# Performance work log

Hardware: AMD Instinct MI355X
Metric: run time of the kernel (lower is better)

Reference implementation:

```python
import jax, jax.numpy as jnp
import numpy as np

N, E, G = 50000, 600000, 64
F_NODE, F_EDGE, F_HAD = 20, 4, 12
D, H, C, L = 128, 4, 32, 3  # hidden, heads, per-head channels, num_layers


def setup_inputs() -> dict:
    key = jax.random.key(0)
    ks = iter(jax.random.split(key, 64))
    nrm = lambda shp, s=0.1: jax.random.normal(next(ks), shp, dtype=jnp.float32) * s
    inp = {
        'x': jax.random.normal(next(ks), (N, F_NODE), dtype=jnp.float32),
        'edge_attr': jax.random.normal(next(ks), (E, F_EDGE), dtype=jnp.float32),
        'haddock_features': jax.random.normal(next(ks), (G, F_HAD), dtype=jnp.float32),
        'edge_index': jax.random.randint(next(ks), (2, E), 0, N, dtype=jnp.int64),
        'batch': (jnp.arange(N, dtype=jnp.int64) * G) // N,  # sorted, all graphs non-empty
        # node embed
        'embed_w': nrm((F_NODE, D)), 'embed_b': jnp.zeros((D,), jnp.float32),
        # GAT layers (stacked over L)
        'gat_lin_w': nrm((L, D, H * C)),
        'gat_att_src': nrm((L, H, C)), 'gat_att_dst': nrm((L, H, C)),
        'gat_edge_w': nrm((L, F_EDGE, H * C)), 'gat_att_edge': nrm((L, H, C)),
        'gat_bias': jnp.zeros((L, H * C), jnp.float32),
        'ln_g': jnp.ones((L, D), jnp.float32), 'ln_b': jnp.zeros((L, D), jnp.float32),
        # haddock processor
        'had_w1': nrm((F_HAD, D)), 'had_b1': jnp.zeros((D,), jnp.float32),
        'had_w2': nrm((D, D)), 'had_b2': jnp.zeros((D,), jnp.float32),
        # interaction head (in = 3*D)
        'int_w1': nrm((3 * D, D)), 'int_b1': jnp.zeros((D,), jnp.float32),
        'int_w2': nrm((D, 64)), 'int_b2': jnp.zeros((64,), jnp.float32),
        'int_w3': nrm((64, 1)), 'int_b3': jnp.zeros((1,), jnp.float32),
        # binding affinity head
        'aff_w1': nrm((3 * D, D)), 'aff_b1': jnp.zeros((D,), jnp.float32),
        'aff_w2': nrm((D, 64)), 'aff_b2': jnp.zeros((64,), jnp.float32),
        'aff_w3': nrm((64, 1)), 'aff_b3': jnp.zeros((1,), jnp.float32),
        # MultiheadAttention with seq_len=1: softmax over 1 key == 1, so output
        # reduces exactly to out_proj(v_proj(x)); q/k projections cancel.
        'mha_v_w': nrm((D, D)), 'mha_v_b': jnp.zeros((D,), jnp.float32),
        'mha_o_w': nrm((D, D)), 'mha_o_b': jnp.zeros((D,), jnp.float32),
    }
    return inp


def _layernorm(x, g, b, eps=1e-5):
    mu = jnp.mean(x, axis=-1, keepdims=True)
    var = jnp.var(x, axis=-1, keepdims=True)
    return (x - mu) * jax.lax.rsqrt(var + eps) * g + b


def _gat_layer(x, src, dst, edge_attr, lin_w, a_src, a_dst, edge_w, a_edge, bias):
    n = x.shape[0]
    h = (x @ lin_w).reshape(n, H, C)                      # [N,H,C]
    alpha_s = jnp.sum(h * a_src, axis=-1)                 # [N,H]
    alpha_d = jnp.sum(h * a_dst, axis=-1)                 # [N,H]
    eemb = (edge_attr @ edge_w).reshape(-1, H, C)         # [E,H,C]
    alpha_e = jnp.sum(eemb * a_edge, axis=-1)             # [E,H]
    alpha = alpha_s[src] + alpha_d[dst] + alpha_e         # [E,H]
    alpha = jax.nn.leaky_relu(alpha, 0.2)
    m = jax.ops.segment_max(alpha, dst, num_segments=n)
    m = jnp.where(jnp.isfinite(m), m, 0.0)
    ex = jnp.exp(alpha - m[dst])
    denom = jax.ops.segment_sum(ex, dst, num_segments=n)
    w = ex / (denom[dst] + 1e-16)                         # segment softmax over dst
    msg = h[src] * w[:, :, None]                          # [E,H,C]
    out = jax.ops.segment_sum(msg, dst, num_segments=n)   # [N,H,C]
    return out.reshape(n, H * C) + bias


def reference(x, edge_attr, haddock_features, embed_w, embed_b,
              gat_lin_w, gat_att_src, gat_att_dst, gat_edge_w, gat_att_edge, gat_bias,
              ln_g, ln_b, had_w1, had_b1, had_w2, had_b2,
              int_w1, int_b1, int_w2, int_b2, int_w3, int_b3,
              aff_w1, aff_b1, aff_w2, aff_b2, aff_w3, aff_b3,
              mha_v_w, mha_v_b, mha_o_w, mha_o_b, edge_index, batch):
    src, dst = edge_index[0], edge_index[1]
    h = jax.nn.relu(x @ embed_w + embed_b)
    for i in range(L):
        res = h
        h = _gat_layer(h, src, dst, edge_attr, gat_lin_w[i], gat_att_src[i],
                       gat_att_dst[i], gat_edge_w[i], gat_att_edge[i], gat_bias[i])
        h = jax.nn.relu(_layernorm(h + res, ln_g[i], ln_b[i]))  # dropout = identity (eval)
    counts = jax.ops.segment_sum(jnp.ones((h.shape[0],), h.dtype), batch, num_segments=G)
    g_mean = jax.ops.segment_sum(h, batch, num_segments=G) / counts[:, None]
    g_max = jax.ops.segment_max(h, batch, num_segments=G)
    graph_embed = jnp.concatenate([g_mean, g_max], axis=1)      # [G,2D]
    had = jax.nn.relu(haddock_features @ had_w1 + had_b1) @ had_w2 + had_b2
    comb = jnp.concatenate([graph_embed, had], axis=1)          # [G,3D]
    z = jax.nn.relu(comb @ int_w1 + int_b1)
    z = jax.nn.relu(z @ int_w2 + int_b2)
    interaction = jax.nn.sigmoid(z @ int_w3 + int_b3)[:, 0]
    z = jax.nn.relu(comb @ aff_w1 + aff_b1)
    z = jax.nn.relu(z @ aff_w2 + aff_b2)
    affinity = (z @ aff_w3 + aff_b3)[:, 0]
    # self-attention over seq_len=1: weights==1, output = out_proj(v_proj(x))
    attn = (h @ mha_v_w + mha_v_b) @ mha_o_w + mha_o_b
    return interaction, affinity, attn, h
```

## Files before the change

### kernel.cpp

```cpp
#include <hip/hip_runtime.h>
#include <hip/hip_bf16.h>

typedef float v4 __attribute__((ext_vector_type(4)));
typedef float f32x4 __attribute__((ext_vector_type(4)));
typedef short bf16x8 __attribute__((ext_vector_type(8)));
typedef unsigned short us8 __attribute__((ext_vector_type(8)));

__device__ __forceinline__ unsigned short f2bf(float f) {
    unsigned u = __float_as_uint(f);
    u = (u + 0x7FFFu + ((u >> 16) & 1u)) >> 16;
    return (unsigned short)u;
}
__device__ __forceinline__ float bf2f(unsigned short s) {
    return __uint_as_float(((unsigned)s) << 16);
}

__global__ __launch_bounds__(256) void k_embed(const float* __restrict__ x,
                                               const float* __restrict__ w,
                                               const float* __restrict__ b,
                                               float* __restrict__ h,
                                               unsigned short* __restrict__ h_bf, int n) {
    int idx = blockIdx.x * 256 + threadIdx.x;
    if (idx >= n * 128) return;
    int node = idx >> 7, j = idx & 127;
    float acc = b[j];
#pragma unroll
    for (int k = 0; k < 20; ++k) acc += x[node * 20 + k] * w[k * 128 + j];
    float r = fmaxf(acc, 0.f);
    h[idx] = r;
    h_bf[idx] = f2bf(r);
}


__global__ __launch_bounds__(256) void k_csr_zero(int* __restrict__ cnt,
                                                  int* __restrict__ cursor, int n) {
    int i = blockIdx.x * 256 + threadIdx.x;
    if (i < n) { cnt[i] = 0; cursor[i] = 0; }
}

__global__ __launch_bounds__(256) void k_hist(const int* __restrict__ ei,
                                              int* __restrict__ cnt, int E_) {
    int e = blockIdx.x * 256 + threadIdx.x;
    if (e < E_) atomicAdd(&cnt[ei[E_ + e]], 1);
}

__global__ __launch_bounds__(256) void k_scan_local(const int* __restrict__ cnt,
                                                    int* __restrict__ ptr,
                                                    int* __restrict__ bsum, int n) {
    __shared__ int s[256];
    int t = threadIdx.x, i = blockIdx.x * 256 + t;
    int v = (i < n) ? cnt[i] : 0;
    s[t] = v;
    __syncthreads();
    for (int o = 1; o < 256; o <<= 1) {
        int x = (t >= o) ? s[t - o] : 0;
        __syncthreads();
        s[t] += x;
        __syncthreads();
    }
    if (i < n) ptr[i] = s[t] - v;
    if (t == 255) bsum[blockIdx.x] = s[255];
}

__global__ __launch_bounds__(256) void k_scan_bsum(int* __restrict__ bsum, int nb) {
    __shared__ int s[256];
    int t = threadIdx.x;
    int v = (t < nb) ? bsum[t] : 0;
    s[t] = v;
    __syncthreads();
    for (int o = 1; o < 256; o <<= 1) {
        int x = (t >= o) ? s[t - o] : 0;
        __syncthreads();
        s[t] += x;
        __syncthreads();
    }
    if (t < nb) bsum[t] = s[t] - v;
}

__global__ __launch_bounds__(256) void k_scan_add(int* __restrict__ ptr,
                                                  const int* __restrict__ bsum,
                                                  int n, int E_) {
    int i = blockIdx.x * 256 + threadIdx.x;
    if (i < n) ptr[i] += bsum[i >> 8];
    if (i == 0) ptr[n] = E_;
}

__global__ __launch_bounds__(256) void k_scatter(const int* __restrict__ ei,
                                                 const float* __restrict__ edge_attr,
                                                 const int* __restrict__ ptr,
                                                 int* __restrict__ cursor,
                                                 int* __restrict__ esrc_s,
                                                 float* __restrict__ ea_s, int E_) {
    int e = blockIdx.x * 256 + threadIdx.x;
    if (e >= E_) return;
    int d = ei[E_ + e];
    int p = ptr[d] + atomicAdd(&cursor[d], 1);
    esrc_s[p] = ei[e];
    ((v4*)ea_s)[p] = ((const v4*)edge_attr)[e];
}

__global__ __launch_bounds__(128) void k_fuse_vo(const float* __restrict__ vw,
                                                 const float* __restrict__ vb,
                                                 const float* __restrict__ ow,
                                                 const float* __restrict__ ob,
                                                 float* __restrict__ Wc,
                                                 float* __restrict__ bc) {
    int k = blockIdx.x, j = threadIdx.x;
    float acc = 0.f;
    for (int m = 0; m < 128; ++m) acc += vw[k * 128 + m] * ow[m * 128 + j];
    Wc[k * 128 + j] = acc;
    if (k == 0) {
        float b = ob[j];
        for (int m = 0; m < 128; ++m) b += vb[m] * ow[m * 128 + j];
        bc[j] = b;
    }
}

__global__ __launch_bounds__(256) void k_pack_w(const float* __restrict__ gat_lin_w,
                                                const float* __restrict__ Wc,
                                                unsigned short* __restrict__ Bpack) {
    int m = blockIdx.y;
    const float* W = (m < 3) ? (gat_lin_w + (size_t)m * 16384) : Wc;
    int idx = blockIdx.x * 256 + threadIdx.x;
    int e = idx & 7, l = (idx >> 3) & 63, kb = (idx >> 9) & 3, c = idx >> 11;
    int k = kb * 32 + ((l >> 4) << 3) + e;
    int col = c * 16 + (l & 15);
    Bpack[(size_t)m * 16384 + idx] = f2bf(W[k * 128 + col]);
}

template <bool ALPHAS, bool OUTF32>
__global__ __launch_bounds__(256) void k_gemm_mfma(
    const unsigned short* __restrict__ A,
    const unsigned short* __restrict__ Bpack,
    const float* __restrict__ bias,
    unsigned short* __restrict__ out_bf,
    float* __restrict__ out_f32,
    const float* __restrict__ avs, const float* __restrict__ avd,
    float* __restrict__ asrc, float* __restrict__ adst, int nn) {
    __shared__ float lds[64][132];
    int tid = threadIdx.x;
    int w = tid >> 6, l = tid & 63;
    int row0 = blockIdx.x * 64;
    int arow = row0 + w * 16 + (l & 15);
    int koff = (l >> 4) * 8;

    bf16x8 a[4];
#pragma unroll
    for (int kb = 0; kb < 4; ++kb)
        a[kb] = *(const bf16x8*)&A[(size_t)arow * 128 + kb * 32 + koff];

    const bf16x8* bp = (const bf16x8*)Bpack;
    f32x4 acc[8];
#pragma unroll
    for (int c = 0; c < 8; ++c) {
        f32x4 z = {0.f, 0.f, 0.f, 0.f};
        acc[c] = z;
#pragma unroll
        for (int kb = 0; kb < 4; ++kb)
            acc[c] = __builtin_amdgcn_mfma_f32_16x16x32_bf16(a[kb], bp[(c * 4 + kb) * 64 + l],
                                                             acc[c], 0, 0, 0);
    }

    int colb = l & 15;
    int rowb = w * 16 + (l >> 4) * 4;
#pragma unroll
    for (int c = 0; c < 8; ++c)
#pragma unroll
        for (int r = 0; r < 4; ++r)
            lds[rowb + r][c * 16 + colb] = acc[c][r];
    __syncthreads();

    int rl = tid >> 2, q = tid & 3;
    int gr = row0 + rl;
    if (gr >= nn) return;
    float v[32];
#pragma unroll
    for (int j = 0; j < 8; ++j)
        *(f32x4*)&v[j * 4] = *(const f32x4*)&lds[rl][q * 32 + j * 4];

    if (ALPHAS) {
        float ps = 0.f, pd = 0.f;
#pragma unroll
        for (int j = 0; j < 32; ++j) {
            ps += v[j] * avs[q * 32 + j];
            pd += v[j] * avd[q * 32 + j];
        }
        asrc[(size_t)gr * 4 + q] = ps;
        adst[(size_t)gr * 4 + q] = pd;
    }
    if (OUTF32) {
#pragma unroll
        for (int j = 0; j < 32; ++j) v[j] += bias[q * 32 + j];
#pragma unroll
        for (int j = 0; j < 8; ++j)
            *(f32x4*)&out_f32[(size_t)gr * 128 + q * 32 + j * 4] = *(f32x4*)&v[j * 4];
    } else {
        us8 o0, o1;
#pragma unroll
        for (int j = 0; j < 8; ++j) o0[j] = f2bf(v[j]);
#pragma unroll
        for (int j = 0; j < 8; ++j) o1[j] = f2bf(v[8 + j]);
        *(us8*)&out_bf[(size_t)gr * 128 + q * 32] = o0;
        *(us8*)&out_bf[(size_t)gr * 128 + q * 32 + 8] = o1;
        us8 o2, o3;
#pragma unroll
        for (int j = 0; j < 8; ++j) o2[j] = f2bf(v[16 + j]);
#pragma unroll
        for (int j = 0; j < 8; ++j) o3[j] = f2bf(v[24 + j]);
        *(us8*)&out_bf[(size_t)gr * 128 + q * 32 + 16] = o2;
        *(us8*)&out_bf[(size_t)gr * 128 + q * 32 + 24] = o3;
    }
}

__global__ __launch_bounds__(256) void k_node_agg(
    const unsigned short* __restrict__ hl_bf, const int* __restrict__ ptr,
    const int* __restrict__ esrc_s, const float* __restrict__ ea_s,
    const float* __restrict__ asrc, const float* __restrict__ adst,
    const float* __restrict__ edge_w, const float* __restrict__ a_edge,
    const float* __restrict__ bias, const float* __restrict__ lng,
    const float* __restrict__ lnb, float* __restrict__ h,
    unsigned short* __restrict__ h_bf, int n) {
    __shared__ float aew[16];
    int tid = threadIdx.x;
    if (tid < 16) {
        int k = tid >> 2, hh = tid & 3;
        float s = 0.f;
        for (int c = 0; c < 32; ++c) s += edge_w[k * 128 + hh * 32 + c] * a_edge[hh * 32 + c];
        aew[tid] = s;
    }
    __syncthreads();

    int node = blockIdx.x * 4 + (tid >> 6);
    if (node >= n) return;
    int lane = tid & 63;
    int g = lane >> 4;
    int l16 = lane & 15;
    int c0 = l16 * 8;
    int hh = l16 >> 2;

    float aewc0 = aew[hh], aewc1 = aew[4 + hh], aewc2 = aew[8 + hh], aewc3 = aew[12 + hh];
    int start = ptr[node], end = ptr[node + 1];
    float adn = adst[(size_t)node * 4 + hh];

    float acc[8] = {};
    float den = 0.f;
    int p = start + g;
    int srcp = (p < end) ? esrc_s[p] : 0;
    for (; p < end; p += 4) {
        int srcn = (p + 4 < end) ? esrc_s[p + 4] : 0;
        v4 ea = ((const v4*)ea_s)[p];
        float a = asrc[(size_t)srcp * 4 + hh] + adn +
                  ea[0] * aewc0 + ea[1] * aewc1 + ea[2] * aewc2 + ea[3] * aewc3;
        a = a > 0.f ? a : 0.2f * a;
        float ex = __expf(a);
        den += ex;
        us8 hv = *(const us8*)&hl_bf[(size_t)srcp * 128 + c0];
#pragma unroll
        for (int j = 0; j < 8; ++j) acc[j] += ex * bf2f(hv[j]);
        srcp = srcn;
    }

#pragma unroll
    for (int j = 0; j < 8; ++j) {
        acc[j] += __shfl_xor(acc[j], 16);
        acc[j] += __shfl_xor(acc[j], 32);
    }
    den += __shfl_xor(den, 16);
    den += __shfl_xor(den, 32);

    float inv = 1.f / (den + 1e-16f);
    v4 r0 = *(const v4*)&h[(size_t)node * 128 + c0];
    v4 r1 = *(const v4*)&h[(size_t)node * 128 + c0 + 4];
    v4 b0 = *(const v4*)&bias[c0];
    v4 b1 = *(const v4*)&bias[c0 + 4];
    float v[8];
#pragma unroll
    for (int j = 0; j < 4; ++j) v[j] = acc[j] * inv + b0[j] + r0[j];
#pragma unroll
    for (int j = 0; j < 4; ++j) v[4 + j] = acc[4 + j] * inv + b1[j] + r1[j];

    float s = 0.f, sq = 0.f;
#pragma unroll
    for (int j = 0; j < 8; ++j) { s += v[j]; sq += v[j] * v[j]; }
#pragma unroll
    for (int o = 1; o < 16; o <<= 1) { s += __shfl_xor(s, o); sq += __shfl_xor(sq, o); }
    float mu = s * (1.f / 128.f);
    float var = sq * (1.f / 128.f) - mu * mu;
    float rs = rsqrtf(var + 1e-5f);

    if (g == 0) {
        v4 g0 = *(const v4*)&lng[c0];
        v4 g1 = *(const v4*)&lng[c0 + 4];
        v4 lb0 = *(const v4*)&lnb[c0];
        v4 lb1 = *(const v4*)&lnb[c0 + 4];
        v4 o0, o1;
#pragma unroll
        for (int j = 0; j < 4; ++j) o0[j] = fmaxf((v[j] - mu) * rs * g0[j] + lb0[j], 0.f);
#pragma unroll
        for (int j = 0; j < 4; ++j) o1[j] = fmaxf((v[4 + j] - mu) * rs * g1[j] + lb1[j], 0.f);
        *(v4*)&h[(size_t)node * 128 + c0] = o0;
        *(v4*)&h[(size_t)node * 128 + c0 + 4] = o1;
        us8 ob;
#pragma unroll
        for (int j = 0; j < 4; ++j) ob[j] = f2bf(o0[j]);
#pragma unroll
        for (int j = 0; j < 4; ++j) ob[4 + j] = f2bf(o1[j]);
        *(us8*)&h_bf[(size_t)node * 128 + c0] = ob;
    }
}

__device__ __forceinline__ int lower_bound_i(const int* a, int n, int key) {
    int lo = 0, hi = n;
    while (lo < hi) {
        int mid = (lo + hi) >> 1;
        if (a[mid] < key) lo = mid + 1; else hi = mid;
    }
    return lo;
}


__global__ __launch_bounds__(256) void k_pool_zero(float* __restrict__ gsum,
                                                   float* __restrict__ gmax, int g128) {
    int i = blockIdx.x * 256 + threadIdx.x;
    if (i < g128) { gsum[i] = 0.f; gmax[i] = 0.f; }
}

__global__ __launch_bounds__(256) void k_pool_part(const float* __restrict__ h,
                                                   const int* __restrict__ batch,
                                                   float* __restrict__ gsum,
                                                   float* __restrict__ gmax,
                                                   int n, int chunk) {
    int start = blockIdx.x * chunk;
    int end = min(start + chunk, n);
    if (start >= end) return;
    int j = threadIdx.x & 127, half = threadIdx.x >> 7;
    float s = 0.f, mx = 0.f;
    int curg = -1;
    for (int node = start + half; node < end; node += 2) {
        int g = batch[node];
        if (g != curg) {
            if (curg >= 0) {
                atomicAdd(&gsum[curg * 128 + j], s);
                atomicMax((int*)&gmax[curg * 128 + j], __float_as_int(mx));
            }
            curg = g; s = 0.f; mx = 0.f;
        }
        float v = h[(size_t)node * 128 + j];
        s += v;
        mx = fmaxf(mx, v);
    }
    if (curg >= 0) {
        atomicAdd(&gsum[curg * 128 + j], s);
        atomicMax((int*)&gmax[curg * 128 + j], __float_as_int(mx));
    }
}

__global__ __launch_bounds__(128) void k_pool_fin(const float* __restrict__ gsum,
                                                  const float* __restrict__ gmax,
                                                  const int* __restrict__ batch,
                                                  float* __restrict__ comb, int n) {
    int g = blockIdx.x, j = threadIdx.x;
    int start = lower_bound_i(batch, n, g);
    int end = lower_bound_i(batch, n, g + 1);
    float cnt = (float)(end - start);
    comb[g * 384 + j] = gsum[g * 128 + j] / cnt;
    comb[g * 384 + 128 + j] = gmax[g * 128 + j];
}

__global__ __launch_bounds__(128) void k_had(const float* __restrict__ hf,
                                             const float* __restrict__ w1,
                                             const float* __restrict__ b1,
                                             const float* __restrict__ w2,
                                             const float* __restrict__ b2,
                                             float* __restrict__ comb) {
    __shared__ float h1[128];
    int g = blockIdx.x, j = threadIdx.x;
    float acc = b1[j];
#pragma unroll
    for (int k = 0; k < 12; ++k) acc += hf[g * 12 + k] * w1[k * 128 + j];
    h1[j] = fmaxf(acc, 0.f);
    __syncthreads();
    float a2 = b2[j];
    for (int k = 0; k < 128; ++k) a2 += h1[k] * w2[k * 128 + j];
    comb[g * 384 + 256 + j] = a2;
}

__global__ __launch_bounds__(128) void k_head(const float* __restrict__ comb,
                                              const float* __restrict__ w1,
                                              const float* __restrict__ b1,
                                              const float* __restrict__ w2,
                                              const float* __restrict__ b2,
                                              const float* __restrict__ w3,
                                              const float* __restrict__ b3,
                                              float* __restrict__ outp, int sigm) {
    __shared__ float cs[384];
    __shared__ float z1[128];
    __shared__ float z2[64];
    int g = blockIdx.x, j = threadIdx.x;
    for (int k = j; k < 384; k += 128) cs[k] = comb[g * 384 + k];
    __syncthreads();
    float acc = b1[j];
    for (int k = 0; k < 384; ++k) acc += cs[k] * w1[k * 128 + j];
    z1[j] = fmaxf(acc, 0.f);
    __syncthreads();
    if (j < 64) {
        float a2 = b2[j];
        for (int k = 0; k < 128; ++k) a2 += z1[k] * w2[k * 64 + j];
        z2[j] = fmaxf(a2, 0.f);
    }
    __syncthreads();
    if (j == 0) {
        float a3 = b3[0];
        for (int k = 0; k < 64; ++k) a3 += z2[k] * w3[k];
        if (sigm) a3 = 1.f / (1.f + __expf(-a3));
        outp[g] = a3;
    }
}

extern "C" void kernel_launch(void* const* d_in, const int* in_sizes, int n_in,
                              void* d_out, int out_size, void* d_ws, size_t ws_size,
                              hipStream_t stream) {
    const float* x = (const float*)d_in[0];
    const float* edge_attr = (const float*)d_in[1];
    const float* haddock = (const float*)d_in[2];
    const int* ei = (const int*)d_in[3];
    const int* batch = (const int*)d_in[4];
    const float* embed_w = (const float*)d_in[5];
    const float* embed_b = (const float*)d_in[6];
    const float* gat_lin_w = (const float*)d_in[7];
    const float* gat_att_src = (const float*)d_in[8];
    const float* gat_att_dst = (const float*)d_in[9];
    const float* gat_edge_w = (const float*)d_in[10];
    const float* gat_att_edge = (const float*)d_in[11];
    const float* gat_bias = (const float*)d_in[12];
    const float* ln_g = (const float*)d_in[13];
    const float* ln_b = (const float*)d_in[14];
    const float* had_w1 = (const float*)d_in[15];
    const float* had_b1 = (const float*)d_in[16];
    const float* had_w2 = (const float*)d_in[17];
    const float* had_b2 = (const float*)d_in[18];
    const float* int_w1 = (const float*)d_in[19];
    const float* int_b1 = (const float*)d_in[20];
    const float* int_w2 = (const float*)d_in[21];
    const float* int_b2 = (const float*)d_in[22];
    const float* int_w3 = (const float*)d_in[23];
    const float* int_b3 = (const float*)d_in[24];
    const float* aff_w1 = (const float*)d_in[25];
    const float* aff_b1 = (const float*)d_in[26];
    const float* aff_w2 = (const float*)d_in[27];
    const float* aff_b2 = (const float*)d_in[28];
    const float* aff_w3 = (const float*)d_in[29];
    const float* aff_b3 = (const float*)d_in[30];
    const float* mha_v_w = (const float*)d_in[31];
    const float* mha_v_b = (const float*)d_in[32];
    const float* mha_o_w = (const float*)d_in[33];
    const float* mha_o_b = (const float*)d_in[34];

    const int N_ = in_sizes[0] / 20;
    const int E_ = in_sizes[1] / 4;
    const int G_ = in_sizes[2] / 12;
    const int Npad = (N_ + 63) & ~63;

    float* out_f = (float*)d_out;
    float* inter_out = out_f;
    float* aff_out = out_f + G_;
    float* attn_out = out_f + 2 * G_;
    float* h_buf = attn_out + (size_t)N_ * 128;

    unsigned short* h_bf = (unsigned short*)d_ws;
    unsigned short* hl_bf = h_bf + (size_t)Npad * 128;
    unsigned short* Bpack = hl_bf + (size_t)Npad * 128;
    float* ea_s = (float*)(Bpack + 4 * 16384);
    float* Wc = ea_s + (size_t)E_ * 4;
    float* bc = Wc + 16384;
    float* asrc = bc + 128;
    float* adst = asrc + (size_t)N_ * 4;
    float* gsum = adst + (size_t)N_ * 4;
    float* gmax = gsum + (size_t)G_ * 128;
    float* comb = gmax + (size_t)G_ * 128;
    int* cnt = (int*)(comb + (size_t)G_ * 384);
    int* cursor = cnt + N_;
    int* ptr = cursor + N_;
    int* bsum = ptr + N_ + 4;
    int* esrc_s = bsum + 256;

    const int nb_scan = (N_ + 255) / 256;
    const int POOL_BLOCKS = 2048;
    const int chunk = (N_ + POOL_BLOCKS - 1) / POOL_BLOCKS;
    const int gemm_blocks = (N_ + 63) / 64;

    k_embed<<<(N_ * 128 + 255) / 256, 256, 0, stream>>>(x, embed_w, embed_b, h_buf, h_bf, N_);

    k_csr_zero<<<nb_scan, 256, 0, stream>>>(cnt, cursor, N_);
    k_hist<<<(E_ + 255) / 256, 256, 0, stream>>>(ei, cnt, E_);
    k_scan_local<<<nb_scan, 256, 0, stream>>>(cnt, ptr, bsum, N_);
    k_scan_bsum<<<1, 256, 0, stream>>>(bsum, nb_scan);
    k_scan_add<<<nb_scan, 256, 0, stream>>>(ptr, bsum, N_, E_);
    k_scatter<<<(E_ + 255) / 256, 256, 0, stream>>>(ei, edge_attr, ptr, cursor,
                                                    esrc_s, ea_s, E_);

    k_fuse_vo<<<128, 128, 0, stream>>>(mha_v_w, mha_v_b, mha_o_w, mha_o_b, Wc, bc);
    k_pack_w<<<dim3(64, 4), 256, 0, stream>>>(gat_lin_w, Wc, Bpack);
    k_pool_zero<<<(G_ * 128 + 255) / 256, 256, 0, stream>>>(gsum, gmax, G_ * 128);

    for (int i = 0; i < 3; ++i) {
        k_gemm_mfma<true, false><<<gemm_blocks, 256, 0, stream>>>(
            h_bf, Bpack + (size_t)i * 16384, nullptr, hl_bf, nullptr,
            gat_att_src + i * 128, gat_att_dst + i * 128, asrc, adst, N_);
        k_node_agg<<<(N_ + 3) / 4, 256, 0, stream>>>(
            hl_bf, ptr, esrc_s, ea_s, asrc, adst,
            gat_edge_w + (size_t)i * 512, gat_att_edge + i * 128,
            gat_bias + i * 128, ln_g + i * 128, ln_b + i * 128, h_buf, h_bf, N_);
    }

    k_pool_part<<<POOL_BLOCKS, 256, 0, stream>>>(h_buf, batch, gsum, gmax, N_, chunk);
    k_pool_fin<<<G_, 128, 0, stream>>>(gsum, gmax, batch, comb, N_);
    k_had<<<G_, 128, 0, stream>>>(haddock, had_w1, had_b1, had_w2, had_b2, comb);
    k_head<<<G_, 128, 0, stream>>>(comb, int_w1, int_b1, int_w2, int_b2, int_w3, int_b3,
                                   inter_out, 1);
    k_head<<<G_, 128, 0, stream>>>(comb, aff_w1, aff_b1, aff_w2, aff_b2, aff_w3, aff_b3,
                                   aff_out, 0);
    k_gemm_mfma<false, true><<<gemm_blocks, 256, 0, stream>>>(
        h_bf, Bpack + (size_t)3 * 16384, bc, nullptr, attn_out,
        nullptr, nullptr, nullptr, nullptr, N_);
}
```

Baseline: 404.8 us.

## Widen node aggregation lanes, fuse graph head kernels, pool from bf16, use memsets

The node aggregation kernel now gives each lane 16 channels and runs 8 edge streams per node instead of 4, so each lane issues wider gathers and more edges are in flight. The pool-finish, haddock and two head kernels are merged into one graph-output kernel. Pooling now reads the bf16 copy of h, which halves its read traffic but may shift results slightly. The zeroing kernels are replaced with hipMemsetAsync, which cuts launch count.

```diff
diff --git a/kernel.cpp b/kernel.cpp
--- a/kernel.cpp
+++ b/kernel.cpp
@@ -31,12 +31,6 @@
     h_bf[idx] = f2bf(r);
 }
 
-
-__global__ __launch_bounds__(256) void k_csr_zero(int* __restrict__ cnt,
-                                                  int* __restrict__ cursor, int n) {
-    int i = blockIdx.x * 256 + threadIdx.x;
-    if (i < n) { cnt[i] = 0; cursor[i] = 0; }
-}
 
 __global__ __launch_bounds__(256) void k_hist(const int* __restrict__ ei,
                                               int* __restrict__ cnt, int E_) {
@@ -195,20 +189,14 @@
         for (int j = 0; j < 8; ++j)
             *(f32x4*)&out_f32[(size_t)gr * 128 + q * 32 + j * 4] = *(f32x4*)&v[j * 4];
     } else {
-        us8 o0, o1;
-#pragma unroll
-        for (int j = 0; j < 8; ++j) o0[j] = f2bf(v[j]);
-#pragma unroll
-        for (int j = 0; j < 8; ++j) o1[j] = f2bf(v[8 + j]);
-        *(us8*)&out_bf[(size_t)gr * 128 + q * 32] = o0;
-        *(us8*)&out_bf[(size_t)gr * 128 + q * 32 + 8] = o1;
-        us8 o2, o3;
-#pragma unroll
-        for (int j = 0; j < 8; ++j) o2[j] = f2bf(v[16 + j]);
-#pragma unroll
-        for (int j = 0; j < 8; ++j) o3[j] = f2bf(v[24 + j]);
-        *(us8*)&out_bf[(size_t)gr * 128 + q * 32 + 16] = o2;
-        *(us8*)&out_bf[(size_t)gr * 128 + q * 32 + 24] = o3;
+        us8 o[4];
+#pragma unroll
+        for (int t = 0; t < 4; ++t)
+#pragma unroll
+            for (int j = 0; j < 8; ++j) o[t][j] = f2bf(v[t * 8 + j]);
+#pragma unroll
+        for (int t = 0; t < 4; ++t)
+            *(us8*)&out_bf[(size_t)gr * 128 + q * 32 + t * 8] = o[t];
     }
 }
 
@@ -233,79 +221,86 @@
     int node = blockIdx.x * 4 + (tid >> 6);
     if (node >= n) return;
     int lane = tid & 63;
-    int g = lane >> 4;
-    int l16 = lane & 15;
-    int c0 = l16 * 8;
-    int hh = l16 >> 2;
+    int g = lane >> 3;
+    int l8 = lane & 7;
+    int c0 = l8 * 16;
+    int hh = l8 >> 1;
 
     float aewc0 = aew[hh], aewc1 = aew[4 + hh], aewc2 = aew[8 + hh], aewc3 = aew[12 + hh];
     int start = ptr[node], end = ptr[node + 1];
     float adn = adst[(size_t)node * 4 + hh];
 
-    float acc[8] = {};
+    float acc[16] = {};
     float den = 0.f;
     int p = start + g;
     int srcp = (p < end) ? esrc_s[p] : 0;
-    for (; p < end; p += 4) {
-        int srcn = (p + 4 < end) ? esrc_s[p + 4] : 0;
+    for (; p < end; p += 8) {
+        int srcn = (p + 8 < end) ? esrc_s[p + 8] : 0;
         v4 ea = ((const v4*)ea_s)[p];
+        us8 hv0 = *(const us8*)&hl_bf[(size_t)srcp * 128 + c0];
+        us8 hv1 = *(const us8*)&hl_bf[(size_t)srcp * 128 + c0 + 8];
         float a = asrc[(size_t)srcp * 4 + hh] + adn +
                   ea[0] * aewc0 + ea[1] * aewc1 + ea[2] * aewc2 + ea[3] * aewc3;
         a = a > 0.f ? a : 0.2f * a;
         float ex = __expf(a);
         den += ex;
-        us8 hv = *(const us8*)&hl_bf[(size_t)srcp * 128 + c0];
-#pragma unroll
-        for (int j = 0; j < 8; ++j) acc[j] += ex * bf2f(hv[j]);
+#pragma unroll
+        for (int j = 0; j < 8; ++j) acc[j] += ex * bf2f(hv0[j]);
+#pragma unroll
+        for (int j = 0; j < 8; ++j) acc[8 + j] += ex * bf2f(hv1[j]);
         srcp = srcn;
     }
 
 #pragma unroll
-    for (int j = 0; j < 8; ++j) {
+    for (int j = 0; j < 16; ++j) {
+        acc[j] += __shfl_xor(acc[j], 8);
         acc[j] += __shfl_xor(acc[j], 16);
         acc[j] += __shfl_xor(acc[j], 32);
     }
+    den += __shfl_xor(den, 8);
     den += __shfl_xor(den, 16);
     den += __shfl_xor(den, 32);
 
     float inv = 1.f / (den + 1e-16f);
-    v4 r0 = *(const v4*)&h[(size_t)node * 128 + c0];
-    v4 r1 = *(const v4*)&h[(size_t)node * 128 + c0 + 4];
-    v4 b0 = *(const v4*)&bias[c0];
-    v4 b1 = *(const v4*)&bias[c0 + 4];
-    float v[8];
-#pragma unroll
-    for (int j = 0; j < 4; ++j) v[j] = acc[j] * inv + b0[j] + r0[j];
-#pragma unroll
-    for (int j = 0; j < 4; ++j) v[4 + j] = acc[4 + j] * inv + b1[j] + r1[j];
+    float v[16];
+#pragma unroll
+    for (int t = 0; t < 4; ++t) {
+        v4 r = *(const v4*)&h[(size_t)node * 128 + c0 + t * 4];
+        v4 b = *(const v4*)&bias[c0 + t * 4];
+#pragma unroll
+        for (int j = 0; j < 4; ++j) v[t * 4 + j] = acc[t * 4 + j] * inv + b[j] + r[j];
+    }
 
     float s = 0.f, sq = 0.f;
 #pragma unroll
-    for (int j = 0; j < 8; ++j) { s += v[j]; sq += v[j] * v[j]; }
-#pragma unroll
-    for (int o = 1; o < 16; o <<= 1) { s += __shfl_xor(s, o); sq += __shfl_xor(sq, o); }
+    for (int j = 0; j < 16; ++j) { s += v[j]; sq += v[j] * v[j]; }
+#pragma unroll
+    for (int o = 1; o < 8; o <<= 1) { s += __shfl_xor(s, o); sq += __shfl_xor(sq, o); }
     float mu = s * (1.f / 128.f);
     float var = sq * (1.f / 128.f) - mu * mu;
     float rs = rsqrtf(var + 1e-5f);
 
     if (g == 0) {
-        v4 g0 = *(const v4*)&lng[c0];
-        v4 g1 = *(const v4*)&lng[c0 + 4];
-        v4 lb0 = *(const v4*)&lnb[c0];
-        v4 lb1 = *(const v4*)&lnb[c0 + 4];
-        v4 o0, o1;
-#pragma unroll
-        for (int j = 0; j < 4; ++j) o0[j] = fmaxf((v[j] - mu) * rs * g0[j] + lb0[j], 0.f);
-#pragma unroll
-        for (int j = 0; j < 4; ++j) o1[j] = fmaxf((v[4 + j] - mu) * rs * g1[j] + lb1[j], 0.f);
-        *(v4*)&h[(size_t)node * 128 + c0] = o0;
-        *(v4*)&h[(size_t)node * 128 + c0 + 4] = o1;
-        us8 ob;
-#pragma unroll
-        for (int j = 0; j < 4; ++j) ob[j] = f2bf(o0[j]);
-#pragma unroll
-        for (int j = 0; j < 4; ++j) ob[4 + j] = f2bf(o1[j]);
-        *(us8*)&h_bf[(size_t)node * 128 + c0] = ob;
+        float y[16];
+#pragma unroll
+        for (int t = 0; t < 4; ++t) {
+            v4 gg = *(const v4*)&lng[c0 + t * 4];
+            v4 lb = *(const v4*)&lnb[c0 + t * 4];
+            v4 o;
+#pragma unroll
+            for (int j = 0; j < 4; ++j) {
+                o[j] = fmaxf((v[t * 4 + j] - mu) * rs * gg[j] + lb[j], 0.f);
+                y[t * 4 + j] = o[j];
+            }
+            *(v4*)&h[(size_t)node * 128 + c0 + t * 4] = o;
+        }
+        us8 ob0, ob1;
+#pragma unroll
+        for (int j = 0; j < 8; ++j) ob0[j] = f2bf(y[j]);
+#pragma unroll
+        for (int j = 0; j < 8; ++j) ob1[j] = f2bf(y[8 + j]);
+        *(us8*)&h_bf[(size_t)node * 128 + c0] = ob0;
+        *(us8*)&h_bf[(size_t)node * 128 + c0 + 8] = ob1;
     }
 }
 
@@ -319,13 +314,7 @@
 }
 
 
-__global__ __launch_bounds__(256) void k_pool_zero(float* __restrict__ gsum,
-                                                   float* __restrict__ gmax, int g128) {
-    int i = blockIdx.x * 256 + threadIdx.x;
-    if (i < g128) { gsum[i] = 0.f; gmax[i] = 0.f; }
-}
-
-__global__ __launch_bounds__(256) void k_pool_part(const float* __restrict__ h,
+__global__ __launch_bounds__(256) void k_pool_part(const unsigned short* __restrict__ h_bf,
                                                    const int* __restrict__ batch,
                                                    float* __restrict__ gsum,
                                                    float* __restrict__ gmax,
@@ -333,87 +322,92 @@
     int start = blockIdx.x * chunk;
     int end = min(start + chunk, n);
     if (start >= end) return;
-    int j = threadIdx.x & 127, half = threadIdx.x >> 7;
-    float s = 0.f, mx = 0.f;
+    int c0 = (threadIdx.x & 63) * 2;
+    int strm = threadIdx.x >> 6;
+    float s0 = 0.f, s1 = 0.f, m0 = 0.f, m1 = 0.f;
     int curg = -1;
-    for (int node = start + half; node < end; node += 2) {
+    for (int node = start + strm; node < end; node += 4) {
         int g = batch[node];
         if (g != curg) {
             if (curg >= 0) {
-                atomicAdd(&gsum[curg * 128 + j], s);
-                atomicMax((int*)&gmax[curg * 128 + j], __float_as_int(mx));
+                atomicAdd(&gsum[curg * 128 + c0], s0);
+                atomicAdd(&gsum[curg * 128 + c0 + 1], s1);
+                atomicMax((int*)&gmax[curg * 128 + c0], __float_as_int(m0));
+                atomicMax((int*)&gmax[curg * 128 + c0 + 1], __float_as_int(m1));
             }
-            curg = g; s = 0.f; mx = 0.f;
+            curg = g; s0 = s1 = 0.f; m0 = m1 = 0.f;
         }
-        float v = h[(size_t)node * 128 + j];
-        s += v;
-        mx = fmaxf(mx, v);
+        unsigned u = *(const unsigned*)&h_bf[(size_t)node * 128 + c0];
+        float v0 = __uint_as_float(u << 16);
+        float v1 = __uint_as_float(u & 0xffff0000u);
+        s0 += v0; s1 += v1;
+        m0 = fmaxf(m0, v0); m1 = fmaxf(m1, v1);
     }
     if (curg >= 0) {
-        atomicAdd(&gsum[curg * 128 + j], s);
-        atomicMax((int*)&gmax[curg * 128 + j], __float_as_int(mx));
-    }
-}
-
-__global__ __launch_bounds__(128) void k_pool_fin(const float* __restrict__ gsum,
-                                                  const float* __restrict__ gmax,
-                                                  const int* __restrict__ batch,
-                                                  float* __restrict__ comb, int n) {
-    int g = blockIdx.x, j = threadIdx.x;
-    int start = lower_bound_i(batch, n, g);
-    int end = lower_bound_i(batch, n, g + 1);
-    float cnt = (float)(end - start);
-    comb[g * 384 + j] = gsum[g * 128 + j] / cnt;
-    comb[g * 384 + 128 + j] = gmax[g * 128 + j];
-}
-
-__global__ __launch_bounds__(128) void k_had(const float* __restrict__ hf,
-                                             const float* __restrict__ w1,
-                                             const float* __restrict__ b1,
-                                             const float* __restrict__ w2,
-                                             const float* __restrict__ b2,
-                                             float* __restrict__ comb) {
+        atomicAdd(&gsum[curg * 128 + c0], s0);
+        atomicAdd(&gsum[curg * 128 + c0 + 1], s1);
+        atomicMax((int*)&gmax[curg * 128 + c0], __float_as_int(m0));
+        atomicMax((int*)&gmax[curg * 128 + c0 + 1], __float_as_int(m1));
+    }
+}
+
+__global__ __launch_bounds__(256) void k_graph_out(
+    const float* __restrict__ gsum, const float* __restrict__ gmax,
+    const int* __restrict__ batch, const float* __restrict__ hf,
+    const float* __restrict__ had_w1, const float* __restrict__ had_b1,
+    const float* __restrict__ had_w2, const float* __restrict__ had_b2,
+    const float* __restrict__ int_w1, const float* __restrict__ int_b1,
+    const float* __restrict__ int_w2, const float* __restrict__ int_b2,
+    const float* __restrict__ int_w3, const float* __restrict__ int_b3,
+    const float* __restrict__ aff_w1, const float* __restrict__ aff_b1,
+    const float* __restrict__ aff_w2, const float* __restrict__ aff_b2,
+    const float* __restrict__ aff_w3, const float* __restrict__ aff_b3,
+    float* __restrict__ inter_out, float* __restrict__ aff_out, int n) {
+    __shared__ float comb[384];
     __shared__ float h1[128];
-    int g = blockIdx.x, j = threadIdx.x;
+    __shared__ float z1[2][128];
+    __shared__ float z2[2][64];
+    int g = blockIdx.x, tid = threadIdx.x;
+    if (tid < 128) {
+        int start = lower_bound_i(batch, n, g);
+        int end = lower_bound_i(batch, n, g + 1);
+        float cnt = (float)(end - start);
+        comb[tid] = gsum[g * 128 + tid] / cnt;
+        comb[128 + tid] = gmax[g * 128 + tid];
+        float acc = had_b1[tid];
+#pragma unroll
+        for (int k = 0; k < 12; ++k) acc += hf[g * 12 + k] * had_w1[k * 128 + tid];
+        h1[tid] = fmaxf(acc, 0.f);
+    }
+    __syncthreads();
+    if (tid < 128) {
+        float a2 = had_b2[tid];
+        for (int k = 0; k < 128; ++k) a2 += h1[k] * had_w2[k * 128 + tid];
+        comb[256 + tid] = a2;
+    }
+    __syncthreads();
+    int hsel = tid >> 7, j = tid & 127;
+    const float* w1 = hsel ? aff_w1 : int_w1;
+    const float* b1 = hsel ? aff_b1 : int_b1;
+    const float* w2 = hsel ? aff_w2 : int_w2;
+    const float* b2 = hsel ? aff_b2 : int_b2;
+    const float* w3 = hsel ? aff_w3 : int_w3;
+    const float* b3 = hsel ? aff_b3 : int_b3;
     float acc = b1[j];
-#pragma unroll
-    for (int k = 0; k < 12; ++k) acc += hf[g * 12 + k] * w1[k * 128 + j];
-    h1[j] = fmaxf(acc, 0.f);
-    __syncthreads();
-    float a2 = b2[j];
-    for (int k = 0; k < 128; ++k) a2 += h1[k] * w2[k * 128 + j];
-    comb[g * 384 + 256 + j] = a2;
-}
-
-__global__ __launch_bounds__(128) void k_head(const float* __restrict__ comb,
-                                              const float* __restrict__ w1,
-                                              const float* __restrict__ b1,
-                                              const float* __restrict__ w2,
-                                              const float* __restrict__ b2,
-                                              const float* __restrict__ w3,
-                                              const float* __restrict__ b3,
-                                              float* __restrict__ outp, int sigm) {
-    __shared__ float cs[384];
-    __shared__ float z1[128];
-    __shared__ float z2[64];
-    int g = blockIdx.x, j = threadIdx.x;
-    for (int k = j; k < 384; k += 128) cs[k] = comb[g * 384 + k];
-    __syncthreads();
-    float acc = b1[j];
-    for (int k = 0; k < 384; ++k) acc += cs[k] * w1[k * 128 + j];
-    z1[j] = fmaxf(acc, 0.f);
+    for (int k = 0; k < 384; ++k) acc += comb[k] * w1[k * 128 + j];
+    z1[hsel][j] = fmaxf(acc, 0.f);
     __syncthreads();
     if (j < 64) {
         float a2 = b2[j];
-        for (int k = 0; k < 128; ++k) a2 += z1[k] * w2[k * 64 + j];
-        z2[j] = fmaxf(a2, 0.f);
+        for (int k = 0; k < 128; ++k) a2 += z1[hsel][k] * w2[k * 64 + j];
+        z2[hsel][j] = fmaxf(a2, 0.f);
     }
     __syncthreads();
     if (j == 0) {
         float a3 = b3[0];
-        for (int k = 0; k < 64; ++k) a3 += z2[k] * w3[k];
-        if (sigm) a3 = 1.f / (1.f + __expf(-a3));
-        outp[g] = a3;
+        for (int k = 0; k < 64; ++k) a3 += z2[hsel][k] * w3[k];
+        if (hsel) aff_out[g] = a3;
+        else inter_out[g] = 1.f / (1.f + __expf(-a3));
     }
 }
 
@@ -477,8 +471,7 @@
     float* adst = asrc + (size_t)N_ * 4;
     float* gsum = adst + (size_t)N_ * 4;
     float* gmax = gsum + (size_t)G_ * 128;
-    float* comb = gmax + (size_t)G_ * 128;
-    int* cnt = (int*)(comb + (size_t)G_ * 384);
+    int* cnt = (int*)(gmax + (size_t)G_ * 128);
     int* cursor = cnt + N_;
     int* ptr = cursor + N_;
     int* bsum = ptr + N_ + 4;
@@ -491,7 +484,7 @@
 
     k_embed<<<(N_ * 128 + 255) / 256, 256, 0, stream>>>(x, embed_w, embed_b, h_buf, h_bf, N_);
 
-    k_csr_zero<<<nb_scan, 256, 0, stream>>>(cnt, cursor, N_);
+    hipMemsetAsync(cnt, 0, (size_t)2 * N_ * sizeof(int), stream);
     k_hist<<<(E_ + 255) / 256, 256, 0, stream>>>(ei, cnt, E_);
     k_scan_local<<<nb_scan, 256, 0, stream>>>(cnt, ptr, bsum, N_);
     k_scan_bsum<<<1, 256, 0, stream>>>(bsum, nb_scan);
@@ -501,7 +494,7 @@
 
     k_fuse_vo<<<128, 128, 0, stream>>>(mha_v_w, mha_v_b, mha_o_w, mha_o_b, Wc, bc);
     k_pack_w<<<dim3(64, 4), 256, 0, stream>>>(gat_lin_w, Wc, Bpack);
-    k_pool_zero<<<(G_ * 128 + 255) / 256, 256, 0, stream>>>(gsum, gmax, G_ * 128);
+    hipMemsetAsync(gsum, 0, (size_t)2 * G_ * 128 * sizeof(float), stream);
 
     for (int i = 0; i < 3; ++i) {
         k_gemm_mfma<true, false><<<gemm_blocks, 256, 0, stream>>>(
@@ -513,13 +506,12 @@
             gat_bias + i * 128, ln_g + i * 128, ln_b + i * 128, h_buf, h_bf, N_);
     }
 
-    k_pool_part<<<POOL_BLOCKS, 256, 0, stream>>>(h_buf, batch, gsum, gmax, N_, chunk);
-    k_pool_fin<<<G_, 128, 0, stream>>>(gsum, gmax, batch, comb, N_);
-    k_had<<<G_, 128, 0, stream>>>(haddock, had_w1, had_b1, had_w2, had_b2, comb);
-    k_head<<<G_, 128, 0, stream>>>(comb, int_w1, int_b1, int_w2, int_b2, int_w3, int_b3,
-                                   inter_out, 1);
-    k_head<<<G_, 128, 0, stream>>>(comb, aff_w1, aff_b1, aff_w2, aff_b2, aff_w3, aff_b3,
-                                   aff_out, 0);
+    k_pool_part<<<POOL_BLOCKS, 256, 0, stream>>>(h_bf, batch, gsum, gmax, N_, chunk);
+    k_graph_out<<<G_, 256, 0, stream>>>(gsum, gmax, batch, haddock,
+                                        had_w1, had_b1, had_w2, had_b2,
+                                        int_w1, int_b1, int_w2, int_b2, int_w3, int_b3,
+                                        aff_w1, aff_b1, aff_w2, aff_b2, aff_w3, aff_b3,
+                                        inter_out, aff_out, N_);
     k_gemm_mfma<false, true><<<gemm_blocks, 256, 0, stream>>>(
         h_bf, Bpack + (size_t)3 * 16384, bc, nullptr, attn_out,
         nullptr, nullptr, nullptr, nullptr, N_);
```

Result: slower. 460.7 us (+13.8%).
